# Optimization experiments

Hardware: AMD Instinct MI355X
Metric: run time of the kernel (lower is better)

Reference implementation:

```python
import jax, jax.numpy as jnp
import numpy as np

BS = 128  # quantization block size


def _dequant(w, s, bs):
    # w: [E, O, I]; s: [E, O//bs, I//bs] block scales -> broadcast to full weight
    return w * jnp.repeat(jnp.repeat(s, bs, axis=1), bs, axis=2)


def setup_inputs() -> dict:
    key = jax.random.key(0)
    ks = jax.random.split(key, 9)
    T, H, I, E, K = 512, 2048, 1024, 16, 4
    x = jax.random.normal(ks[0], (T, H), dtype=jnp.float32)
    w0 = jax.random.normal(ks[1], (E, I, H), dtype=jnp.float32) * 0.02
    w1 = jax.random.normal(ks[2], (E, I, H), dtype=jnp.float32) * 0.02
    w2 = jax.random.normal(ks[3], (E, H, I), dtype=jnp.float32) * 0.02
    s0 = jax.random.uniform(ks[4], (E, I // BS, H // BS), dtype=jnp.float32) + 0.5
    s1 = jax.random.uniform(ks[5], (E, I // BS, H // BS), dtype=jnp.float32) + 0.5
    s2 = jax.random.uniform(ks[6], (E, H // BS, I // BS), dtype=jnp.float32) + 0.5
    selected_experts = jax.random.randint(ks[7], (T, K), 0, E, dtype=jnp.int64)
    routing_weights = jax.random.uniform(ks[8], (T, K), dtype=jnp.float32)
    return {"x": x, "w0": w0, "w1": w1, "w2": w2, "s0": s0, "s1": s1,
            "s2": s2, "selected_experts": selected_experts,
            "routing_weights": routing_weights}


def reference(x, w0, w1, w2, s0, s1, s2, selected_experts, routing_weights):
    # Dequantize block-quantized expert weights
    w0d = _dequant(w0, s0, BS)  # [E, I, H] gate proj
    w1d = _dequant(w1, s1, BS)  # [E, I, H] up proj
    w2d = _dequant(w2, s2, BS)  # [E, H, I] down proj
    # SwiGLU FFN for every (token, expert) pair via batched GEMMs
    g = jnp.einsum('th,eih->tei', x, w0d)          # [T, E, I]
    u = jnp.einsum('th,eih->tei', x, w1d)          # [T, E, I]
    h = jax.nn.silu(g) * u                          # [T, E, I]
    y = jnp.einsum('tei,ehi->teh', h, w2d)          # [T, E, H]
    # Gather the top-k selected experts per token and weight them
    idx = selected_experts[:, :, None]              # [T, K, 1]
    y_sel = jnp.take_along_axis(y, idx, axis=1)     # [T, K, H]
    out = y_sel * routing_weights[:, :, None]       # [T, K, H]
    return out
```

## Files before the change

### kernel.cpp

```cpp
#include <hip/hip_runtime.h>
#include <math.h>

#define T_DIM 512
#define H_DIM 2048
#define I_DIM 1024
#define E_DIM 16
#define NP    2048
#define BM    64
#define MAXCH 48
#define LIST_OFF 256
#define HWS_OFF  4096
#define BK    128
#define LDK   136

typedef float  float4v __attribute__((ext_vector_type(4)));
typedef short  short8v __attribute__((ext_vector_type(8)));

__device__ __forceinline__ unsigned int bfr(float f) {
    unsigned int u = __builtin_bit_cast(unsigned int, f);
    return (u + 0x7fffu + ((u >> 16) & 1u)) >> 16;
}
__device__ __forceinline__ unsigned int pk2(float a, float b) {
    return bfr(a) | (bfr(b) << 16);
}

__global__ void count_kernel(const int* __restrict__ sel, int* __restrict__ meta) {
    int p = blockIdx.x * 256 + threadIdx.x;
    if (p < NP) atomicAdd(&meta[sel[p]], 1);
}

__global__ void plan_kernel(int* __restrict__ meta) {
    if (threadIdx.x != 0 || blockIdx.x != 0) return;
    int off = 0, ci = 0;
    for (int e = 0; e < E_DIM; ++e) {
        int c = meta[e];
        meta[16 + e] = off;
        int nch = (c + BM - 1) / BM;
        for (int j = 0; j < nch; ++j) meta[32 + ci++] = e;
        off += nch * BM;
    }
    for (; ci < MAXCH; ++ci) meta[32 + ci] = -1;
}

__global__ void scatter_kernel(const int* __restrict__ sel, int* __restrict__ meta) {
    int p = blockIdx.x * 256 + threadIdx.x;
    if (p < NP) {
        int e = sel[p];
        int pos = atomicAdd(&meta[16 + e], 1);
        meta[LIST_OFF + pos] = p;
    }
}

__global__ __launch_bounds__(256, 3) void gemm01_kernel(
    const float* __restrict__ x, const float* __restrict__ w0g,
    const float* __restrict__ w1g, const float* __restrict__ s0,
    const float* __restrict__ s1, const int* __restrict__ meta,
    unsigned short* __restrict__ hbuf) {
    int e = meta[32 + blockIdx.x];
    if (e < 0) return;
    int itile = blockIdx.y;
    int tid = threadIdx.x;

    __shared__ unsigned short xs[BM][LDK];
    __shared__ unsigned short as[BM][LDK];
    __shared__ unsigned short bs[BM][LDK];
    __shared__ int prow[BM];
    __shared__ int trow[BM];

    if (tid < BM) {
        int p = meta[LIST_OFF + blockIdx.x * BM + tid];
        prow[tid] = p;
        trow[tid] = p >= 0 ? (p >> 2) : 0;
    }
    __syncthreads();

    const int lane = tid & 63;
    const int wid  = tid >> 6;
    const int l15  = lane & 15;
    const int kq   = (lane >> 4) * 8;
    const int ib   = itile >> 1;

    float4v zero = {0.f, 0.f, 0.f, 0.f};
    float4v accg[4], accu[4];
#pragma unroll
    for (int t = 0; t < 4; ++t) { accg[t] = zero; accu[t] = zero; }

    const int r  = tid >> 2;
    const int c0 = tid & 3;
    const float* xrow  = x   + (size_t)trow[r] * H_DIM;
    const float* w0row = w0g + ((size_t)e * I_DIM + itile * 64 + r) * H_DIM;
    const float* w1row = w1g + ((size_t)e * I_DIM + itile * 64 + r) * H_DIM;

    for (int hb = 0; hb < H_DIM / BK; ++hb) {
        float sg = s0[((size_t)e * (I_DIM/128) + ib) * (H_DIM/128) + hb];
        float su = s1[((size_t)e * (I_DIM/128) + ib) * (H_DIM/128) + hb];
        const int h0 = hb * BK;
#pragma unroll
        for (int q = 0; q < 8; ++q) {
            int c4 = (c0 + q * 4) * 4;
            float4 v = *(const float4*)(xrow + h0 + c4);
            *(uint2*)&xs[r][c4] = make_uint2(pk2(v.x, v.y), pk2(v.z, v.w));
        }
#pragma unroll
        for (int q = 0; q < 8; ++q) {
            int c4 = (c0 + q * 4) * 4;
            float4 v = *(const float4*)(w0row + h0 + c4);
            *(uint2*)&as[r][c4] = make_uint2(pk2(v.x * sg, v.y * sg), pk2(v.z * sg, v.w * sg));
        }
#pragma unroll
        for (int q = 0; q < 8; ++q) {
            int c4 = (c0 + q * 4) * 4;
            float4 v = *(const float4*)(w1row + h0 + c4);
            *(uint2*)&bs[r][c4] = make_uint2(pk2(v.x * su, v.y * su), pk2(v.z * su, v.w * su));
        }
        __syncthreads();
#pragma unroll
        for (int ks = 0; ks < BK / 32; ++ks) {
            int koff = ks * 32 + kq;
            short8v af = *(const short8v*)&xs[wid * 16 + l15][koff];
#pragma unroll
            for (int nt = 0; nt < 4; ++nt) {
                short8v b0 = *(const short8v*)&as[nt * 16 + l15][koff];
                accg[nt] = __builtin_amdgcn_mfma_f32_16x16x32_bf16(af, b0, accg[nt], 0, 0, 0);
                short8v b1 = *(const short8v*)&bs[nt * 16 + l15][koff];
                accu[nt] = __builtin_amdgcn_mfma_f32_16x16x32_bf16(af, b1, accu[nt], 0, 0, 0);
            }
        }
        __syncthreads();
    }

    int rowb = wid * 16 + (lane >> 4) * 4;
    int colb = itile * 64 + l15;
#pragma unroll
    for (int nt = 0; nt < 4; ++nt) {
#pragma unroll
        for (int rg = 0; rg < 4; ++rg) {
            int p = prow[rowb + rg];
            if (p < 0) continue;
            float g = accg[nt][rg], u = accu[nt][rg];
            float h = g / (1.f + __expf(-g)) * u;
            hbuf[(size_t)p * I_DIM + colb + nt * 16] = (unsigned short)bfr(h);
        }
    }
}

__global__ __launch_bounds__(256, 4) void gemm2_kernel(
    const unsigned short* __restrict__ hbuf, const float* __restrict__ w2g,
    const float* __restrict__ s2, const float* __restrict__ rw,
    const int* __restrict__ meta, float* __restrict__ out) {
    int e = meta[32 + blockIdx.x];
    if (e < 0) return;
    int htile = blockIdx.y;
    int tid = threadIdx.x;

    __shared__ unsigned short hs[BM][LDK];
    __shared__ unsigned short wsm[BM][LDK];
    __shared__ int prow[BM];

    if (tid < BM) prow[tid] = meta[LIST_OFF + blockIdx.x * BM + tid];
    __syncthreads();

    const int lane = tid & 63;
    const int wid  = tid >> 6;
    const int l15  = lane & 15;
    const int kq   = (lane >> 4) * 8;
    const int hbk  = htile >> 1;

    float4v zero = {0.f, 0.f, 0.f, 0.f};
    float4v acc[4];
#pragma unroll
    for (int t = 0; t < 4; ++t) acc[t] = zero;

    const int r  = tid >> 2;
    const int c0 = tid & 3;
    int pr = prow[r]; if (pr < 0) pr = 0;
    const unsigned short* hrow = hbuf + (size_t)pr * I_DIM;
    const float* wrow = w2g + ((size_t)e * H_DIM + htile * 64 + r) * I_DIM;

    for (int ibk = 0; ibk < I_DIM / BK; ++ibk) {
        float sc = s2[((size_t)e * (H_DIM/128) + hbk) * (I_DIM/128) + ibk];
        const int i0 = ibk * BK;
#pragma unroll
        for (int q = 0; q < 8; ++q) {
            int c4 = (c0 + q * 4) * 4;
            *(uint2*)&hs[r][c4] = *(const uint2*)(hrow + i0 + c4);
        }
#pragma unroll
        for (int q = 0; q < 8; ++q) {
            int c4 = (c0 + q * 4) * 4;
            float4 v = *(const float4*)(wrow + i0 + c4);
            *(uint2*)&wsm[r][c4] = make_uint2(pk2(v.x * sc, v.y * sc), pk2(v.z * sc, v.w * sc));
        }
        __syncthreads();
#pragma unroll
        for (int ks = 0; ks < BK / 32; ++ks) {
            int koff = ks * 32 + kq;
            short8v af = *(const short8v*)&hs[wid * 16 + l15][koff];
#pragma unroll
            for (int nt = 0; nt < 4; ++nt) {
                short8v bfv = *(const short8v*)&wsm[nt * 16 + l15][koff];
                acc[nt] = __builtin_amdgcn_mfma_f32_16x16x32_bf16(af, bfv, acc[nt], 0, 0, 0);
            }
        }
        __syncthreads();
    }

    int rowb = wid * 16 + (lane >> 4) * 4;
    int colb = htile * 64 + l15;
#pragma unroll
    for (int nt = 0; nt < 4; ++nt) {
#pragma unroll
        for (int rg = 0; rg < 4; ++rg) {
            int p = prow[rowb + rg];
            if (p < 0) continue;
            out[(size_t)p * H_DIM + colb + nt * 16] = acc[nt][rg] * rw[p];
        }
    }
}

extern "C" void kernel_launch(void* const* d_in, const int* in_sizes, int n_in,
                              void* d_out, int out_size, void* d_ws, size_t ws_size,
                              hipStream_t stream) {
    const float* x  = (const float*)d_in[0];
    const float* w0 = (const float*)d_in[1];
    const float* w1 = (const float*)d_in[2];
    const float* w2 = (const float*)d_in[3];
    const float* s0 = (const float*)d_in[4];
    const float* s1 = (const float*)d_in[5];
    const float* s2 = (const float*)d_in[6];
    const int* sel  = (const int*)d_in[7];
    const float* rw = (const float*)d_in[8];
    float* out = (float*)d_out;
    int* meta = (int*)d_ws;
    unsigned short* hbuf = (unsigned short*)((float*)d_ws + HWS_OFF);

    hipMemsetAsync(meta, 0, 16 * sizeof(int), stream);
    hipMemsetAsync(meta + LIST_OFF, 0xFF, MAXCH * BM * sizeof(int), stream);
    count_kernel<<<NP / 256, 256, 0, stream>>>(sel, meta);
    plan_kernel<<<1, 64, 0, stream>>>(meta);
    scatter_kernel<<<NP / 256, 256, 0, stream>>>(sel, meta);
    gemm01_kernel<<<dim3(MAXCH, I_DIM / 64), 256, 0, stream>>>(x, w0, w1, s0, s1, meta, hbuf);
    gemm2_kernel<<<dim3(MAXCH, H_DIM / 64), 256, 0, stream>>>(hbuf, w2, s2, rw, meta, out);
}
```

Measured before the change: 464.0 us.

## Fuse routing into one kernel, prefetch GEMM tiles into registers, swap grid axes

```diff
diff --git a/kernel.cpp b/kernel.cpp
--- a/kernel.cpp
+++ b/kernel.cpp
@@ -24,41 +24,44 @@
     return bfr(a) | (bfr(b) << 16);
 }
 
-__global__ void count_kernel(const int* __restrict__ sel, int* __restrict__ meta) {
-    int p = blockIdx.x * 256 + threadIdx.x;
-    if (p < NP) atomicAdd(&meta[sel[p]], 1);
-}
-
-__global__ void plan_kernel(int* __restrict__ meta) {
-    if (threadIdx.x != 0 || blockIdx.x != 0) return;
-    int off = 0, ci = 0;
-    for (int e = 0; e < E_DIM; ++e) {
-        int c = meta[e];
-        meta[16 + e] = off;
-        int nch = (c + BM - 1) / BM;
-        for (int j = 0; j < nch; ++j) meta[32 + ci++] = e;
-        off += nch * BM;
-    }
-    for (; ci < MAXCH; ++ci) meta[32 + ci] = -1;
-}
-
-__global__ void scatter_kernel(const int* __restrict__ sel, int* __restrict__ meta) {
-    int p = blockIdx.x * 256 + threadIdx.x;
-    if (p < NP) {
-        int e = sel[p];
-        int pos = atomicAdd(&meta[16 + e], 1);
-        meta[LIST_OFF + pos] = p;
-    }
-}
-
-__global__ __launch_bounds__(256, 3) void gemm01_kernel(
+__global__ __launch_bounds__(1024) void route_kernel(const int* __restrict__ sel,
+                                                     int* __restrict__ meta) {
+    __shared__ int cnt[E_DIM];
+    __shared__ int wptr[E_DIM];
+    int tid = threadIdx.x;
+    if (tid < E_DIM) cnt[tid] = 0;
+    __syncthreads();
+    int p0 = tid, p1 = tid + 1024;
+    int e0 = sel[p0], e1 = sel[p1];
+    atomicAdd(&cnt[e0], 1);
+    atomicAdd(&cnt[e1], 1);
+    for (int i = tid; i < MAXCH * BM; i += 1024) meta[LIST_OFF + i] = -1;
+    __syncthreads();
+    if (tid == 0) {
+        int off = 0, ci = 0;
+        for (int e = 0; e < E_DIM; ++e) {
+            wptr[e] = off;
+            int nch = (cnt[e] + BM - 1) / BM;
+            for (int j = 0; j < nch; ++j) meta[32 + ci++] = e;
+            off += nch * BM;
+        }
+        for (; ci < MAXCH; ++ci) meta[32 + ci] = -1;
+    }
+    __syncthreads();
+    int pos0 = atomicAdd(&wptr[e0], 1);
+    meta[LIST_OFF + pos0] = p0;
+    int pos1 = atomicAdd(&wptr[e1], 1);
+    meta[LIST_OFF + pos1] = p1;
+}
+
+__global__ __launch_bounds__(256, 2) void gemm01_kernel(
     const float* __restrict__ x, const float* __restrict__ w0g,
     const float* __restrict__ w1g, const float* __restrict__ s0,
     const float* __restrict__ s1, const int* __restrict__ meta,
     unsigned short* __restrict__ hbuf) {
-    int e = meta[32 + blockIdx.x];
+    int e = meta[32 + blockIdx.y];
     if (e < 0) return;
-    int itile = blockIdx.y;
+    int itile = blockIdx.x;
     int tid = threadIdx.x;
 
     __shared__ unsigned short xs[BM][LDK];
@@ -68,7 +71,7 @@
     __shared__ int trow[BM];
 
     if (tid < BM) {
-        int p = meta[LIST_OFF + blockIdx.x * BM + tid];
+        int p = meta[LIST_OFF + blockIdx.y * BM + tid];
         prow[tid] = p;
         trow[tid] = p >= 0 ? (p >> 2) : 0;
     }
@@ -90,30 +93,41 @@
     const float* xrow  = x   + (size_t)trow[r] * H_DIM;
     const float* w0row = w0g + ((size_t)e * I_DIM + itile * 64 + r) * H_DIM;
     const float* w1row = w1g + ((size_t)e * I_DIM + itile * 64 + r) * H_DIM;
+    const float* s0p = s0 + ((size_t)e * (I_DIM/128) + ib) * (H_DIM/128);
+    const float* s1p = s1 + ((size_t)e * (I_DIM/128) + ib) * (H_DIM/128);
+
+    float4 px[8], pa[8], pb[8];
+#pragma unroll
+    for (int q = 0; q < 8; ++q) {
+        int c4 = (c0 + q * 4) * 4;
+        px[q] = *(const float4*)(xrow + c4);
+        pa[q] = *(const float4*)(w0row + c4);
+        pb[q] = *(const float4*)(w1row + c4);
+    }
 
     for (int hb = 0; hb < H_DIM / BK; ++hb) {
-        float sg = s0[((size_t)e * (I_DIM/128) + ib) * (H_DIM/128) + hb];
-        float su = s1[((size_t)e * (I_DIM/128) + ib) * (H_DIM/128) + hb];
-        const int h0 = hb * BK;
+        float sg = s0p[hb];
+        float su = s1p[hb];
 #pragma unroll
         for (int q = 0; q < 8; ++q) {
             int c4 = (c0 + q * 4) * 4;
-            float4 v = *(const float4*)(xrow + h0 + c4);
-            *(uint2*)&xs[r][c4] = make_uint2(pk2(v.x, v.y), pk2(v.z, v.w));
-        }
-#pragma unroll
-        for (int q = 0; q < 8; ++q) {
-            int c4 = (c0 + q * 4) * 4;
-            float4 v = *(const float4*)(w0row + h0 + c4);
-            *(uint2*)&as[r][c4] = make_uint2(pk2(v.x * sg, v.y * sg), pk2(v.z * sg, v.w * sg));
-        }
-#pragma unroll
-        for (int q = 0; q < 8; ++q) {
-            int c4 = (c0 + q * 4) * 4;
-            float4 v = *(const float4*)(w1row + h0 + c4);
-            *(uint2*)&bs[r][c4] = make_uint2(pk2(v.x * su, v.y * su), pk2(v.z * su, v.w * su));
-        }
-        __syncthreads();
+            *(uint2*)&xs[r][c4] = make_uint2(pk2(px[q].x, px[q].y), pk2(px[q].z, px[q].w));
+            *(uint2*)&as[r][c4] = make_uint2(pk2(pa[q].x * sg, pa[q].y * sg),
+                                             pk2(pa[q].z * sg, pa[q].w * sg));
+            *(uint2*)&bs[r][c4] = make_uint2(pk2(pb[q].x * su, pb[q].y * su),
+                                             pk2(pb[q].z * su, pb[q].w * su));
+        }
+        __syncthreads();
+        if (hb + 1 < H_DIM / BK) {
+            const int h0 = (hb + 1) * BK;
+#pragma unroll
+            for (int q = 0; q < 8; ++q) {
+                int c4 = (c0 + q * 4) * 4;
+                px[q] = *(const float4*)(xrow + h0 + c4);
+                pa[q] = *(const float4*)(w0row + h0 + c4);
+                pb[q] = *(const float4*)(w1row + h0 + c4);
+            }
+        }
 #pragma unroll
         for (int ks = 0; ks < BK / 32; ++ks) {
             int koff = ks * 32 + kq;
@@ -144,20 +158,20 @@
     }
 }
 
-__global__ __launch_bounds__(256, 4) void gemm2_kernel(
+__global__ __launch_bounds__(256, 3) void gemm2_kernel(
     const unsigned short* __restrict__ hbuf, const float* __restrict__ w2g,
     const float* __restrict__ s2, const float* __restrict__ rw,
     const int* __restrict__ meta, float* __restrict__ out) {
-    int e = meta[32 + blockIdx.x];
+    int e = meta[32 + blockIdx.y];
     if (e < 0) return;
-    int htile = blockIdx.y;
+    int htile = blockIdx.x;
     int tid = threadIdx.x;
 
     __shared__ unsigned short hs[BM][LDK];
     __shared__ unsigned short wsm[BM][LDK];
     __shared__ int prow[BM];
 
-    if (tid < BM) prow[tid] = meta[LIST_OFF + blockIdx.x * BM + tid];
+    if (tid < BM) prow[tid] = meta[LIST_OFF + blockIdx.y * BM + tid];
     __syncthreads();
 
     const int lane = tid & 63;
@@ -176,22 +190,36 @@
     int pr = prow[r]; if (pr < 0) pr = 0;
     const unsigned short* hrow = hbuf + (size_t)pr * I_DIM;
     const float* wrow = w2g + ((size_t)e * H_DIM + htile * 64 + r) * I_DIM;
+    const float* s2p = s2 + ((size_t)e * (H_DIM/128) + hbk) * (I_DIM/128);
+
+    uint2  ph[8];
+    float4 pw[8];
+#pragma unroll
+    for (int q = 0; q < 8; ++q) {
+        int c4 = (c0 + q * 4) * 4;
+        ph[q] = *(const uint2*)(hrow + c4);
+        pw[q] = *(const float4*)(wrow + c4);
+    }
 
     for (int ibk = 0; ibk < I_DIM / BK; ++ibk) {
-        float sc = s2[((size_t)e * (H_DIM/128) + hbk) * (I_DIM/128) + ibk];
-        const int i0 = ibk * BK;
+        float sc = s2p[ibk];
 #pragma unroll
         for (int q = 0; q < 8; ++q) {
             int c4 = (c0 + q * 4) * 4;
-            *(uint2*)&hs[r][c4] = *(const uint2*)(hrow + i0 + c4);
-        }
-#pragma unroll
-        for (int q = 0; q < 8; ++q) {
-            int c4 = (c0 + q * 4) * 4;
-            float4 v = *(const float4*)(wrow + i0 + c4);
-            *(uint2*)&wsm[r][c4] = make_uint2(pk2(v.x * sc, v.y * sc), pk2(v.z * sc, v.w * sc));
-        }
-        __syncthreads();
+            *(uint2*)&hs[r][c4] = ph[q];
+            *(uint2*)&wsm[r][c4] = make_uint2(pk2(pw[q].x * sc, pw[q].y * sc),
+                                              pk2(pw[q].z * sc, pw[q].w * sc));
+        }
+        __syncthreads();
+        if (ibk + 1 < I_DIM / BK) {
+            const int i0 = (ibk + 1) * BK;
+#pragma unroll
+            for (int q = 0; q < 8; ++q) {
+                int c4 = (c0 + q * 4) * 4;
+                ph[q] = *(const uint2*)(hrow + i0 + c4);
+                pw[q] = *(const float4*)(wrow + i0 + c4);
+            }
+        }
 #pragma unroll
         for (int ks = 0; ks < BK / 32; ++ks) {
             int koff = ks * 32 + kq;
@@ -234,11 +262,7 @@
     int* meta = (int*)d_ws;
     unsigned short* hbuf = (unsigned short*)((float*)d_ws + HWS_OFF);
 
-    hipMemsetAsync(meta, 0, 16 * sizeof(int), stream);
-    hipMemsetAsync(meta + LIST_OFF, 0xFF, MAXCH * BM * sizeof(int), stream);
-    count_kernel<<<NP / 256, 256, 0, stream>>>(sel, meta);
-    plan_kernel<<<1, 64, 0, stream>>>(meta);
-    scatter_kernel<<<NP / 256, 256, 0, stream>>>(sel, meta);
-    gemm01_kernel<<<dim3(MAXCH, I_DIM / 64), 256, 0, stream>>>(x, w0, w1, s0, s1, meta, hbuf);
-    gemm2_kernel<<<dim3(MAXCH, H_DIM / 64), 256, 0, stream>>>(hbuf, w2, s2, rw, meta, out);
-}
+    route_kernel<<<1, 1024, 0, stream>>>(sel, meta);
+    gemm01_kernel<<<dim3(I_DIM / 64, MAXCH), 256, 0, stream>>>(x, w0, w1, s0, s1, meta, hbuf);
+    gemm2_kernel<<<dim3(H_DIM / 64, MAXCH), 256, 0, stream>>>(hbuf, w2, s2, rw, meta, out);
+}
```

After: 452.1 us. -2.5%, faster.
